# Performance work log

Measured on AMD Instinct MI355X. Metric: run time of the kernel, lower is better.

Reference implementation:

```python
import jax, jax.numpy as jnp
import numpy as np

B, T, C = 4, 1024, 1024
HS = 64
H = C // HS
D_W, D_A, D_V, D_G = 64, 64, 32, 128
EPS = 0.00064  # GroupNorm eps from the module


def _wkv(r, w, k, v, a, b):
    # RWKV-7 recurrence: S_t = S_{t-1}*diag(exp(-exp(w_t))) + (S_{t-1} a_t) b_t^T + v_t k_t^T ; y_t = S_t r_t
    Bv, Tv, Cv = r.shape
    rs = lambda t: t.reshape(Bv, Tv, H, HS)
    r, k, v, a, b = rs(r), rs(k), rs(v), rs(a), rs(b)
    wd = jnp.exp(-jnp.exp(rs(w)))  # per-head per-channel decay in (0,1)

    def step(S, xs):
        r_, w_, k_, v_, a_, b_ = xs  # each (B,H,N)
        sa = jnp.einsum('bhij,bhj->bhi', S, a_)
        S = S * w_[:, :, None, :] + sa[..., None] * b_[:, :, None, :] + v_[..., None] * k_[:, :, None, :]
        y = jnp.einsum('bhij,bhj->bhi', S, r_)
        return S, y

    xs = tuple(jnp.swapaxes(t, 0, 1) for t in (r, wd, k, v, a, b))  # (T,B,H,N)
    S0 = jnp.zeros((Bv, H, HS, HS), r.dtype)
    _, ys = jax.lax.scan(step, S0, xs)
    return jnp.swapaxes(ys, 0, 1).reshape(Bv, Tv, Cv)


def _forward(x, x_r, x_w, x_k, x_v, x_a, x_g, w0, w1, w2, a0, a1, a2, v0, v1, v2,
             g1, g2, k_k, k_a, r_k, Wr, Wk, Wv, Wo, ln_w, ln_b):
    Bv, Tv, Cv = x.shape
    # time_shift(x) - x  (ZeroPad2d((0,0,1,-1)))
    xx = jnp.concatenate([jnp.zeros_like(x[:, :1]), x[:, :-1]], axis=1) - x
    xr = x + xx * x_r; xw = x + xx * x_w; xk = x + xx * x_k
    xv = x + xx * x_v; xa = x + xx * x_a; xg = x + xx * x_g
    r = xr @ Wr
    w = -jax.nn.softplus(-(w0 + jnp.tanh(xw @ w1) @ w2)) - 0.5
    k = xk @ Wk
    v = xv @ Wv
    v_first = jax.lax.stop_gradient(v)  # first layer call: v_first == v.detach()
    v = v + (v_first - v) * jax.nn.sigmoid(v0 + xv @ v1 @ v2)
    a = jax.nn.sigmoid(a0 + xa @ a1 @ a2)
    g = jax.nn.sigmoid(xg @ g1) @ g2
    kk = k * k_k
    kkh = kk.reshape(Bv, Tv, H, HS)
    kkh = kkh / jnp.maximum(jnp.linalg.norm(kkh, axis=-1, keepdims=True), 1e-12)  # F.normalize
    kk = kkh.reshape(Bv, Tv, Cv)
    k = k * (1 + (a - 1) * k_a)
    y = _wkv(r, w, k, v, -kk, kk * a)
    # GroupNorm(H groups, eps=0.00064) over flattened (B*T, C)
    yh = y.reshape(Bv, Tv, H, HS)
    mu = jnp.mean(yh, axis=-1, keepdims=True)
    var = jnp.var(yh, axis=-1, keepdims=True)
    y = ((yh - mu) / jnp.sqrt(var + EPS)).reshape(Bv, Tv, Cv) * ln_w + ln_b
    rt = (r.reshape(Bv, Tv, H, HS) * k.reshape(Bv, Tv, H, HS) * r_k).sum(-1, keepdims=True) * v.reshape(Bv, Tv, H, HS)
    y = y + rt.reshape(Bv, Tv, Cv)
    return (y * g) @ Wo


def setup_inputs():
    key = jax.random.key(0)
    ks = jax.random.split(key, 28)
    it = iter(range(28))
    n = lambda shape, std: jax.random.normal(ks[next(it)], shape, jnp.float32) * std
    s = C ** -0.5
    return {
        'x': n((B, T, C), 1.0),
        'x_r': n((1, 1, C), 0.01), 'x_w': n((1, 1, C), 0.01), 'x_k': n((1, 1, C), 0.01),
        'x_v': n((1, 1, C), 0.01), 'x_a': n((1, 1, C), 0.01), 'x_g': n((1, 1, C), 0.01),
        'w0': n((1, 1, C), 0.02), 'w1': n((C, D_W), 0.04), 'w2': n((D_W, C), 0.04),
        'a0': n((1, 1, C), 0.02), 'a1': n((C, D_A), 0.04), 'a2': n((D_A, C), 0.04),
        'v0': n((1, 1, C), 0.02), 'v1': n((C, D_V), 0.04), 'v2': n((D_V, C), 0.04),
        'g1': n((C, D_G), 0.04), 'g2': n((D_G, C), 0.04),
        'k_k': n((1, 1, C), 0.02), 'k_a': n((1, 1, C), 0.02),
        'r_k': n((H, HS), 0.1) + 0.1 * jnp.arange(H, dtype=jnp.float32)[:, None],
        'Wr': n((C, C), s), 'Wk': n((C, C), s), 'Wv': n((C, C), s), 'Wo': n((C, C), s),
        'ln_w': jnp.ones((C,), jnp.float32), 'ln_b': jnp.zeros((C,), jnp.float32),
    }


def reference(x, x_r, x_w, x_k, x_v, x_a, x_g, w0, w1, w2, a0, a1, a2, v0, v1, v2,
              g1, g2, k_k, k_a, r_k, Wr, Wk, Wv, Wo, ln_w, ln_b):
    return _forward(x, x_r, x_w, x_k, x_v, x_a, x_g, w0, w1, w2, a0, a1, a2,
                    v0, v1, v2, g1, g2, k_k, k_a, r_k, Wr, Wk, Wv, Wo, ln_w, ln_b)
```

## Files before the change

kernel.cpp:

```cpp
#include <hip/hip_runtime.h>
#include <math.h>

#define Bsz 4
#define Tt  1024
#define Cc  1024
#define Hh  16
#define HSs 64
#define CL  32
#define NCH (Tt / CL)
#define STRD 260

typedef __attribute__((ext_vector_type(8))) short bf16x8;
typedef __attribute__((ext_vector_type(4))) float f32x4;

__device__ __forceinline__ float sigf(float x) { return 1.f / (1.f + expf(-x)); }

__device__ __forceinline__ unsigned short f2bf(float f) {
    unsigned int u = __float_as_uint(f);
    u = u + 0x7fffu + ((u >> 16) & 1u);
    return (unsigned short)(u >> 16);
}
__device__ __forceinline__ float bf2f(unsigned short u) {
    return __uint_as_float(((unsigned int)u) << 16);
}
__device__ __forceinline__ float dpp_add_xor1(float x) {
    int y = __builtin_amdgcn_mov_dpp(__float_as_int(x), 0xB1, 0xF, 0xF, true);
    return x + __int_as_float(y);
}
__device__ __forceinline__ float dpp_add_xor2(float x) {
    int y = __builtin_amdgcn_mov_dpp(__float_as_int(x), 0x4E, 0xF, 0xF, true);
    return x + __int_as_float(y);
}

__device__ __forceinline__ void gload16(const void* g, void* l) {
    __builtin_amdgcn_global_load_lds(
        (const __attribute__((address_space(1))) unsigned int*)g,
        (__attribute__((address_space(3))) unsigned int*)l, 16, 0, 0);
}

__device__ __forceinline__ void tcast64(
    const float* __restrict__ W, unsigned short* __restrict__ WT,
    int K, int N, int n0, int k0, int tid, unsigned short tile[64][68])
{
    const int tr = tid >> 4, tc4 = (tid & 15) * 4;
#pragma unroll
    for (int s = 0; s < 4; ++s) {
        int kk = tr + s * 16;
        float4 w4 = *(const float4*)(W + (size_t)(k0 + kk) * N + n0 + tc4);
        tile[kk][tc4 + 0] = f2bf(w4.x);
        tile[kk][tc4 + 1] = f2bf(w4.y);
        tile[kk][tc4 + 2] = f2bf(w4.z);
        tile[kk][tc4 + 3] = f2bf(w4.w);
    }
    __syncthreads();
#pragma unroll
    for (int s = 0; s < 4; ++s) {
        int nn = tr + s * 16;
        ushort4 o4;
        o4.x = tile[tc4 + 0][nn];
        o4.y = tile[tc4 + 1][nn];
        o4.z = tile[tc4 + 2][nn];
        o4.w = tile[tc4 + 3][nn];
        *(ushort4*)(WT + (size_t)(n0 + nn) * K + k0 + tc4) = o4;
    }
}

__global__ __launch_bounds__(256) void prep_all(
    const float* __restrict__ x, const float* __restrict__ x_r,
    const float* __restrict__ x_k, const float* __restrict__ x_v,
    const float* __restrict__ Wr, const float* __restrict__ Wk,
    const float* __restrict__ Wv, const float* __restrict__ Wo,
// ... 34 lines not shown
        for (int j = 0; j < 4; ++j) {
            float xx = xpf[j] - xcf[j];
            rp[j] = f2bf(xcf[j] + xx * mrf[j]);
            kp[j] = f2bf(xcf[j] + xx * mkf[j]);
            vp[j] = f2bf(xcf[j] + xx * mvf[j]);
        }
        *(ushort4*)(xr + o + c0) = r4;
        *(ushort4*)(xk + o + c0) = k4;
        *(ushort4*)(xvo + o + c0) = v4;
        return;
    }
    bid -= 4096;
    if (bid < 1024) {
        int which = bid >> 8, id0 = bid & 255;
        const float* W = which == 0 ? Wr : which == 1 ? Wk : which == 2 ? Wv : Wo;
        unsigned short* WT = which == 0 ? WrT : which == 1 ? WkT : which == 2 ? WvT : WoT;
        tcast64(W, WT, Cc, Cc, (id0 & 15) * 64, (id0 >> 4) * 64, tid, tile);
        return;
    }
    bid -= 1024;
    if (bid < 16) { tcast64(w1, w1t, Cc, 64, 0, bid * 64, tid, tile); return; }
    bid -= 16;
    if (bid < 16) { tcast64(a1, a1t, Cc, 64, 0, bid * 64, tid, tile); return; }
    bid -= 16;
    if (bid < 32) { tcast64(g1, g1t, Cc, 128, (bid & 1) * 64, (bid >> 1) * 64, tid, tile); return; }
    bid -= 32;
    if (bid < 16) { tcast64(w2, w2t, 64, Cc, bid * 64, 0, tid, tile); return; }
    bid -= 16;
    if (bid < 16) { tcast64(a2, a2t, 64, Cc, bid * 64, 0, tid, tile); return; }
    bid -= 16;
    tcast64(g2, g2t, 128, Cc, (bid & 15) * 64, (bid >> 4) * 64, tid, tile);
}

__global__ __launch_bounds__(256) void gemm_rkv(
    const unsigned short* __restrict__ xr, const unsigned short* __restrict__ xk,
    const unsigned short* __restrict__ xv,
    const unsigned short* __restrict__ WrT, const unsigned short* __restrict__ WkT,
    const unsigned short* __restrict__ WvT,
    unsigned short* __restrict__ rbh, float* __restrict__ kb, float* __restrict__ vb)
{
    const int z = blockIdx.z;
    const unsigned short* A  = z == 0 ? xr : z == 1 ? xk : xv;
    const unsigned short* WT = z == 0 ? WrT : z == 1 ? WkT : WvT;
    const int K = Cc, N = Cc;

    __shared__ __attribute__((aligned(16))) unsigned short As[128 * 32];
    __shared__ __attribute__((aligned(16))) unsigned short Bs[128 * 32];
    const int row0 = blockIdx.y * 128;
    const int col0 = blockIdx.x * 128;
    const int tid = threadIdx.x;
    const int wave = tid >> 6, lane = tid & 63;
    const int wr = wave >> 1, wc = wave & 1;
    const int lr = lane & 15, lk = lane >> 4;

    f32x4 acc[4][4];
#pragma unroll
    for (int m = 0; m < 4; ++m)
#pragma unroll
        for (int n = 0; n < 4; ++n)
#pragma unroll
            for (int r = 0; r < 4; ++r) acc[m][n][r] = 0.f;

    const int lrow = lane >> 2;
    const int lcol8 = (lane & 3) * 8;

    for (int k0 = 0; k0 < K; k0 += 32) {
#pragma unroll
        for (int e = 0; e < 2; ++e) {
            int cib = wave * 128 + e * 64;
            int row = (cib >> 2) + lrow;
            gload16(A  + (size_t)(row0 + row) * K + k0 + lcol8, &As[cib * 8]);
            gload16(WT + (size_t)(col0 + row) * K + k0 + lcol8, &Bs[cib * 8]);
        }
        __syncthreads();
        bf16x8 af[4], bff[4];
#pragma unroll
        for (int m = 0; m < 4; ++m)
            af[m] = *(const bf16x8*)&As[(wr * 64 + m * 16 + lr) * 32 + lk * 8];
#pragma unroll
        for (int n = 0; n < 4; ++n)
            bff[n] = *(const bf16x8*)&Bs[(wc * 64 + n * 16 + lr) * 32 + lk * 8];
#pragma unroll
        for (int m = 0; m < 4; ++m)
#pragma unroll
            for (int n = 0; n < 4; ++n)
                acc[m][n] = __builtin_amdgcn_mfma_f32_16x16x32_bf16(af[m], bff[n], acc[m][n], 0, 0, 0);
        __syncthreads();
    }

#pragma unroll
    for (int m = 0; m < 4; ++m)
#pragma unroll
        for (int n = 0; n < 4; ++n) {
            int col = col0 + wc * 64 + n * 16 + lr;
#pragma unroll
            for (int r = 0; r < 4; ++r) {
                int row = row0 + wr * 64 + m * 16 + lk * 4 + r;
                if (z == 0) rbh[(size_t)row * N + col] = f2bf(acc[m][n][r]);
                else if (z == 1) kb[(size_t)row * N + col] = acc[m][n][r];
                else vb[(size_t)row * N + col] = acc[m][n][r];
            }
        }
}

__global__ __launch_bounds__(256) void gemm_bf16(
    const unsigned short* __restrict__ A, const unsigned short* __restrict__ WT,
    float* __restrict__ out, int M, int N, int K)
{
    __shared__ __attribute__((aligned(16))) unsigned short As[128 * 32];
    __shared__ __attribute__((aligned(16))) unsigned short Bs[128 * 32];
    const int row0 = blockIdx.y * 128;
    const int col0 = blockIdx.x * 128;
    const int tid = threadIdx.x;
    const int wave = tid >> 6, lane = tid & 63;
    const int wr = wave >> 1, wc = wave & 1;
    const int lr = lane & 15, lk = lane >> 4;

    f32x4 acc[4][4];
#pragma unroll
    for (int m = 0; m < 4; ++m)
#pragma unroll
        for (int n = 0; n < 4; ++n)
#pragma unroll
            for (int r = 0; r < 4; ++r) acc[m][n][r] = 0.f;

    const int lrow = lane >> 2;
    const int lcol8 = (lane & 3) * 8;

    for (int k0 = 0; k0 < K; k0 += 32) {
#pragma unroll
        for (int e = 0; e < 2; ++e) {
            int cib = wave * 128 + e * 64;
            int row = (cib >> 2) + lrow;
            gload16(A  + (size_t)(row0 + row) * K + k0 + lcol8, &As[cib * 8]);
            gload16(WT + (size_t)(col0 + row) * K + k0 + lcol8, &Bs[cib * 8]);
        }
        __syncthreads();
        bf16x8 af[4], bff[4];
#pragma unroll
        for (int m = 0; m < 4; ++m)
            af[m] = *(const bf16x8*)&As[(wr * 64 + m * 16 + lr) * 32 + lk * 8];
#pragma unroll
        for (int n = 0; n < 4; ++n)
            bff[n] = *(const bf16x8*)&Bs[(wc * 64 + n * 16 + lr) * 32 + lk * 8];
#pragma unroll
        for (int m = 0; m < 4; ++m)
#pragma unroll
            for (int n = 0; n < 4; ++n)
                acc[m][n] = __builtin_amdgcn_mfma_f32_16x16x32_bf16(af[m], bff[n], acc[m][n], 0, 0, 0);
        __syncthreads();
    }

#pragma unroll
    for (int m = 0; m < 4; ++m)
#pragma unroll
        for (int n = 0; n < 4; ++n) {
            int col = col0 + wc * 64 + n * 16 + lr;
#pragma unroll
            for (int r = 0; r < 4; ++r) {
                int row = row0 + wr * 64 + m * 16 + lk * 4 + r;
                out[(size_t)row * N + col] = acc[m][n][r];
            }
        }
}

__global__ __launch_bounds__(256) void lowrank1_fused(
    const float* __restrict__ x,
    const float* __restrict__ x_w, const float* __restrict__ x_a,
    const float* __restrict__ x_g,
    const unsigned short* __restrict__ w1t, const unsigned short* __restrict__ a1t,
    const unsigned short* __restrict__ g1t,
    unsigned short* __restrict__ hw, unsigned short* __restrict__ ha,
    unsigned short* __restrict__ hg)
{
    const int seg = blockIdx.x;
    const float* mix; const unsigned short* WT; unsigned short* out;
    int N, col0, epi;
    if (seg == 0)      { mix = x_w; WT = w1t; out = hw; N = 64;  col0 = 0; epi = 1; }
    else if (seg == 1) { mix = x_a; WT = a1t; out = ha; N = 64;  col0 = 0; epi = 0; }
    else               { mix = x_g; WT = g1t; out = hg; N = 128; col0 = (seg - 2) * 64; epi = 2; }

    __shared__ __attribute__((aligned(16))) unsigned short As[128][40];
    __shared__ __attribute__((aligned(16))) unsigned short Bs[64][40];
    const int row0 = blockIdx.y * 128;
    const int tid = threadIdx.x;
    const int wave = tid >> 6, lane = tid & 63;
    const int lr = lane & 15, lk = lane >> 4;

    f32x4 acc[2][4];
#pragma unroll
    for (int m = 0; m < 2; ++m)
#pragma unroll
        for (int n = 0; n < 4; ++n)
#pragma unroll
            for (int r = 0; r < 4; ++r) acc[m][n][r] = 0.f;

    for (int k0 = 0; k0 < Cc; k0 += 32) {
#pragma unroll
        for (int e = 0; e < 2; ++e) {
            int idx = tid * 2 + e;
            int ar = idx >> 2, ac = (idx & 3) * 8;
            int row = row0 + ar;
            const float* xp = x + (size_t)row * Cc + k0 + ac;
            float4 c0 = *(const float4*)xp;
            float4 c1 = *(const float4*)(xp + 4);
            float4 p0, p1;
            if (row & (Tt - 1)) {
                p0 = *(const float4*)(xp - Cc);
                p1 = *(const float4*)(xp - Cc + 4);
            } else {
                p0.x = p0.y = p0.z = p0.w = 0.f;
                p1.x = p1.y = p1.z = p1.w = 0.f;
            }
            float4 m0 = *(const float4*)(mix + k0 + ac);
            float4 m1 = *(const float4*)(mix + k0 + ac + 4);
            const float* cf0 = (const float*)&c0; const float* cf1 = (const float*)&c1;
            const float* pf0 = (const float*)&p0; const float* pf1 = (const float*)&p1;
            const float* mf0 = (const float*)&m0; const float* mf1 = (const float*)&m1;
            ushort4 u0, u1;
            unsigned short* up0 = (unsigned short*)&u0;
            unsigned short* up1 = (unsigned short*)&u1;
#pragma unroll
            for (int j = 0; j < 4; ++j) {
                up0[j] = f2bf(cf0[j] + (pf0[j] - cf0[j]) * mf0[j]);
                up1[j] = f2bf(cf1[j] + (pf1[j] - cf1[j]) * mf1[j]);
            }
            *(ushort4*)&As[ar][ac] = u0;
            *(ushort4*)&As[ar][ac + 4] = u1;
        }
        {
            int br = tid >> 2, bc = (tid & 3) * 8;
            *(uint4*)&Bs[br][bc] = *(const uint4*)(WT + (size_t)(col0 + br) * Cc + k0 + bc);
        }
        __syncthreads();
        bf16x8 af[2], bff[4];
#pragma unroll
        for (int m = 0; m < 2; ++m)
            af[m] = *(const bf16x8*)&As[wave * 32 + m * 16 + lr][lk * 8];
#pragma unroll
        for (int n = 0; n < 4; ++n)
            bff[n] = *(const bf16x8*)&Bs[n * 16 + lr][lk * 8];
#pragma unroll
        for (int m = 0; m < 2; ++m)
#pragma unroll
            for (int n = 0; n < 4; ++n)
                acc[m][n] = __builtin_amdgcn_mfma_f32_16x16x32_bf16(af[m], bff[n], acc[m][n], 0, 0, 0);
        __syncthreads();
    }

#pragma unroll
    for (int m = 0; m < 2; ++m)
#pragma unroll
        for (int n = 0; n < 4; ++n) {
            int col = col0 + n * 16 + lr;
#pragma unroll
            for (int r = 0; r < 4; ++r) {
                int row = row0 + wave * 32 + m * 16 + lk * 4 + r;
                float v = acc[m][n][r];
                if (epi == 1) v = tanhf(v);
                else if (epi == 2) v = sigf(v);
                out[(size_t)row * N + col] = f2bf(v);
            }
        }
}

__global__ __launch_bounds__(256) void stage2_fused(
    const unsigned short* __restrict__ hw, const unsigned short* __restrict__ ha,
    const unsigned short* __restrict__ hg,
    const unsigned short* __restrict__ w2t, const unsigned short* __restrict__ a2t,
    const unsigned short* __restrict__ g2t,
    unsigned short* __restrict__ wdbh, float* __restrict__ ab,
    unsigned short* __restrict__ gb,
    const float* __restrict__ w0, const float* __restrict__ a0)
{
    const int z = blockIdx.z;
    const unsigned short* A  = z == 0 ? hw : z == 1 ? ha : hg;
    const unsigned short* WT = z == 0 ? w2t : z == 1 ? a2t : g2t;
    const float* bias = z == 0 ? w0 : z == 1 ? a0 : nullptr;
    const int K = (z == 2) ? 128 : 64;
    const int N = Cc;

    __shared__ __attribute__((aligned(16))) unsigned short As[128 * 32];
    __shared__ __attribute__((aligned(16))) unsigned short Bs[64 * 32];
    const int row0 = blockIdx.y * 128;
    const int col0 = blockIdx.x * 64;
    const int tid = threadIdx.x;
    const int wave = tid >> 6, lane = tid & 63;
    const int lr = lane & 15, lk = lane >> 4;

    f32x4 acc[2][4];
#pragma unroll
    for (int m = 0; m < 2; ++m)
#pragma unroll
        for (int n = 0; n < 4; ++n)
// ... 24 lines not shown
        for (int n = 0; n < 4; ++n)
            bff[n] = *(const bf16x8*)&Bs[(n * 16 + lr) * 32 + lk * 8];
#pragma unroll
        for (int m = 0; m < 2; ++m)
#pragma unroll
            for (int n = 0; n < 4; ++n)
                acc[m][n] = __builtin_amdgcn_mfma_f32_16x16x32_bf16(af[m], bff[n], acc[m][n], 0, 0, 0);
        __syncthreads();
    }

#pragma unroll
    for (int m = 0; m < 2; ++m)
#pragma unroll
        for (int n = 0; n < 4; ++n) {
            int col = col0 + n * 16 + lr;
#pragma unroll
            for (int r = 0; r < 4; ++r) {
                int row = row0 + wave * 32 + m * 16 + lk * 4 + r;
                float v = acc[m][n][r];
                if (bias) v += bias[col];
                if (z == 0) {
                    v = expf(-0.60653065971263342f * sigf(v));
                    wdbh[(size_t)row * N + col] = f2bf(v);
                } else if (z == 1) {
                    ab[(size_t)row * N + col] = sigf(v);
                } else {
                    gb[(size_t)row * N + col] = f2bf(v);
                }
            }
        }
}

__global__ __launch_bounds__(256) void prep_k_kernel(
    const float* kraw, const float* __restrict__ a,
    const float* __restrict__ k_k, const float* __restrict__ k_a,
    float* kout, unsigned short* __restrict__ aah, unsigned short* __restrict__ bbh)
{
    const int row = blockIdx.x;
    const int tid = threadIdx.x;
    const int c0 = tid * 4;
    const size_t o = (size_t)row * Cc;

    float4 kr = *(const float4*)(kraw + o + c0);
    float4 kkw = *(const float4*)(k_k + c0);
    float4 av = *(const float4*)(a + o + c0);
    float4 kaw = *(const float4*)(k_a + c0);

    float kk[4] = { kr.x * kkw.x, kr.y * kkw.y, kr.z * kkw.z, kr.w * kkw.w };
    float ssq = kk[0]*kk[0] + kk[1]*kk[1] + kk[2]*kk[2] + kk[3]*kk[3];
    ssq += __shfl_xor(ssq, 1);
    ssq += __shfl_xor(ssq, 2);
    ssq += __shfl_xor(ssq, 4);
    ssq += __shfl_xor(ssq, 8);
    float inv = 1.f / fmaxf(sqrtf(ssq), 1e-12f);

    float krr[4] = { kr.x, kr.y, kr.z, kr.w };
    float av4[4] = { av.x, av.y, av.z, av.w };
    float ka4[4] = { kaw.x, kaw.y, kaw.z, kaw.w };
    ushort4 aa4, bb4;
    unsigned short* aap = (unsigned short*)&aa4;
    unsigned short* bbp = (unsigned short*)&bb4;
    float4 kf4;
    float* kfp = (float*)&kf4;
#pragma unroll
    for (int j = 0; j < 4; ++j) {
        float kkn = kk[j] * inv;
        aap[j] = f2bf(-kkn);
        bbp[j] = f2bf(kkn * av4[j]);
        kfp[j] = krr[j] * (1.f + (av4[j] - 1.f) * ka4[j]);
    }
    *(ushort4*)(aah + o + c0) = aa4;
    *(ushort4*)(bbh + o + c0) = bb4;
    *(float4*)(kout + o + c0) = kf4;
}

__global__ __launch_bounds__(256, 1) void wkv_chunk1(
    const unsigned short* __restrict__ rbh, const unsigned short* __restrict__ wdbh,
    const float* __restrict__ kb,
    const unsigned short* __restrict__ aah, const unsigned short* __restrict__ bbh,
    unsigned short* __restrict__ TLt,
    unsigned short* __restrict__ Rho,
    unsigned short* __restrict__ ZLt,
    unsigned short* __restrict__ Alh)
{
    __shared__ float st[CL * STRD];
    __shared__ float A_l[CL][CL + 1];
    const int blk = blockIdx.x;
    const int bh = blk >> 5;
    const int c  = blk & (NCH - 1);
    const int b = bh >> 4, h = bh & 15;
    const size_t base = (size_t)b * Tt * Cc + h * HSs + (size_t)c * CL * Cc;
    const int tid = threadIdx.x;

    {
        const unsigned short* srcs[4] = { aah, wdbh, bbh, rbh };
        const int s = tid >> 3, j8 = (tid & 7) * 8;
#pragma unroll
        for (int arr = 0; arr < 4; ++arr) {
            uint4 u = *(const uint4*)(srcs[arr] + base + (size_t)s * Cc + j8);
            const unsigned int* q = (const unsigned int*)&u;
            float4 f0, f1;
            f0.x = __uint_as_float(q[0] << 16); f0.y = __uint_as_float(q[0] & 0xFFFF0000u);
            f0.z = __uint_as_float(q[1] << 16); f0.w = __uint_as_float(q[1] & 0xFFFF0000u);
            f1.x = __uint_as_float(q[2] << 16); f1.y = __uint_as_float(q[2] & 0xFFFF0000u);
            f1.z = __uint_as_float(q[3] << 16); f1.w = __uint_as_float(q[3] & 0xFFFF0000u);
            *(float4*)&st[s * STRD + arr * 64 + j8] = f0;
            *(float4*)&st[s * STRD + arr * 64 + j8 + 4] = f1;
        }
    }
    __syncthreads();

// ... 49 lines not shown
                    T[rr][4 + e]  = fmaf(T[rr][4 + e],  w[4 + e],  ta[rr] * bv[4 + e]);
                    T[rr][8 + e]  = fmaf(T[rr][8 + e],  w[8 + e],  ta[rr] * bv[8 + e]);
                    T[rr][12 + e] = fmaf(T[rr][12 + e], w[12 + e], ta[rr] * bv[12 + e]);
                    q0 = fmaf(T[rr][e], r[e], q0);
                    q1 = fmaf(T[rr][4 + e], r[4 + e], q1);
                    q2 = fmaf(T[rr][8 + e], r[8 + e], q2);
                    q3 = fmaf(T[rr][12 + e], r[12 + e], q3);
                }
                rp[rr] = (q0 + q1) + (q2 + q3);
            }
#pragma unroll
            for (int rr = 0; rr < 2; ++rr) {
                rp[rr] = dpp_add_xor1(rp[rr]);
                rp[rr] = dpp_add_xor2(rp[rr]);
            }
            if (jc == 0) {
                ushort2 o2;
                o2.x = f2bf(rp[0]); o2.y = f2bf(rp[1]);
                *(ushort2*)(Rho + rhob + t * 64 + i0) = o2;
            }
        }
        const size_t tlb = (size_t)blk * 4096;
#pragma unroll
        for (int cc = 0; cc < 16; ++cc) {
            ushort2 o2;
            o2.x = f2bf(T[0][cc]); o2.y = f2bf(T[1][cc]);
            *(ushort2*)(TLt + tlb + (size_t)(j0 + cc) * 64 + i0) = o2;
        }
    } else {
        const int idx2 = (wv - 2) * 64 + lane;
        const int s = idx2 >> 2, q4 = idx2 & 3;
        const int j0 = q4 * 16;
        float kreg[16];
#pragma unroll
        for (int q = 0; q < 4; ++q)
            *(float4*)&kreg[q * 4] = *(const float4*)(kb + base + (size_t)s * Cc + j0 + q * 4);
        float z[16];
#pragma unroll
        for (int u = 0; u < 16; ++u) z[u] = 0.f;

        for (int t = 0; t < CL; ++t) {
            const float* sp = st + t * STRD;
            float a[16], w[16], bv[16], r[16];
#pragma unroll
            for (int q = 0; q < 4; ++q) {
                *(float4*)&a[q * 4]  = *(const float4*)(sp + 0 * 64 + j0 + q * 4);
                *(float4*)&w[q * 4]  = *(const float4*)(sp + 1 * 64 + j0 + q * 4);
                *(float4*)&bv[q * 4] = *(const float4*)(sp + 2 * 64 + j0 + q * 4);
                *(float4*)&r[q * 4]  = *(const float4*)(sp + 3 * 64 + j0 + q * 4);
            }
            float q0 = z[0] * a[0], q1 = z[4] * a[4];
            float q2 = z[8] * a[8], q3 = z[12] * a[12];
#pragma unroll
            for (int e = 1; e < 4; ++e) {
                q0 = fmaf(z[e], a[e], q0);
                q1 = fmaf(z[4 + e], a[4 + e], q1);
                q2 = fmaf(z[8 + e], a[8 + e], q2);
                q3 = fmaf(z[12 + e], a[12 + e], q3);
            }
            float za = (q0 + q1) + (q2 + q3);
            za = dpp_add_xor1(za);
            za = dpp_add_xor2(za);
#pragma unroll
            for (int u = 0; u < 16; ++u)
                z[u] = fmaf(z[u], w[u], za * bv[u]);
            if (s == t) {
#pragma unroll
                for (int u = 0; u < 16; ++u) z[u] = kreg[u];
            }
// ... 5 lines not shown
                p1 = fmaf(z[4 + e], r[4 + e], p1);
                p2 = fmaf(z[8 + e], r[8 + e], p2);
                p3 = fmaf(z[12 + e], r[12 + e], p3);
            }
            float al = (p0 + p1) + (p2 + p3);
            al = dpp_add_xor1(al);
            al = dpp_add_xor2(al);
            if (q4 == 0) A_l[t][s] = al;
        }
        const size_t zlb = (size_t)blk * (CL * 64);
#pragma unroll
        for (int u = 0; u < 16; ++u)
            ZLt[zlb + (size_t)(j0 + u) * 32 + s] = f2bf(z[u]);
    }
    __syncthreads();

    if (tid < 128) {
        const int t = tid >> 2, s8 = (tid & 3) * 8;
        ushort4 o0, o1;
        unsigned short* p0 = (unsigned short*)&o0;
        unsigned short* p1 = (unsigned short*)&o1;
#pragma unroll
        for (int e = 0; e < 4; ++e) {
            p0[e] = f2bf(A_l[t][s8 + e]);
            p1[e] = f2bf(A_l[t][s8 + 4 + e]);
        }
        unsigned short* dst = Alh + (size_t)blk * 1024 + t * 32 + s8;
        *(ushort4*)dst = o0;
        *(ushort4*)(dst + 4) = o1;
    }
}

__global__ __launch_bounds__(256, 1) void wkv_chunk2(
    const float* __restrict__ vb, const unsigned short* __restrict__ TLt,
    const unsigned short* __restrict__ Rho, const unsigned short* __restrict__ ZLt,
    const unsigned short* __restrict__ Alh, float* __restrict__ yb)
{
    __shared__ unsigned short Sl[64 * 72];
    __shared__ unsigned short Ttl[64 * 72];
    __shared__ unsigned short Ztl[64 * 40];
    __shared__ unsigned short Rl[32 * 72];
    __shared__ unsigned short Vtl[64 * 40];
    __shared__ unsigned short All[32 * 40];
    const int bh = blockIdx.x;
    const size_t vbase = (size_t)(bh >> 4) * Tt * Cc + (bh & 15) * HSs;
    const int tid = threadIdx.x;
    const int wv = tid >> 6, lane = tid & 63;
    const int lr = lane & 15, lk = lane >> 4;
    const int i0w = wv * 16;

    f32x4 S[4];
#pragma unroll
    for (int n = 0; n < 4; ++n)
#pragma unroll
        for (int r = 0; r < 4; ++r) S[n][r] = 0.f;

    uint4 pT0, pT1, pZ, pR, pAl;
    float4 pV0, pV1;
    const int vs = tid >> 3, vi0 = (tid & 7) * 8;

#define C2_LOAD(c_) do { \
    size_t cb_ = (size_t)(bh * NCH + (c_)); \
    const uint4* tp_ = (const uint4*)(TLt + cb_ * 4096); \
    pT0 = tp_[tid * 2]; pT1 = tp_[tid * 2 + 1]; \
    pZ = ((const uint4*)(ZLt + cb_ * 2048))[tid]; \
    pR = ((const uint4*)(Rho + cb_ * 2048))[tid]; \
    if (tid < 128) pAl = ((const uint4*)(Alh + cb_ * 1024))[tid]; \
    const float* vp_ = vb + vbase + (size_t)((c_) * CL + vs) * Cc + vi0; \
    pV0 = *(const float4*)vp_; pV1 = *(const float4*)(vp_ + 4); \
} while (0)

#define C2_STORE() do { \
    *(uint4*)&Ttl[(tid >> 2) * 72 + (tid & 3) * 16] = pT0; \
    *(uint4*)&Ttl[(tid >> 2) * 72 + (tid & 3) * 16 + 8] = pT1; \
    *(uint4*)&Ztl[(tid >> 2) * 40 + (tid & 3) * 8] = pZ; \
    *(uint4*)&Rl[(tid >> 3) * 72 + (tid & 7) * 8] = pR; \
    if (tid < 128) *(uint4*)&All[(tid >> 2) * 40 + (tid & 3) * 8] = pAl; \
    const float* pv_ = (const float*)&pV0; \
    Vtl[(vi0 + 0) * 40 + vs] = f2bf(pv_[0]); \
    Vtl[(vi0 + 1) * 40 + vs] = f2bf(pv_[1]); \
    Vtl[(vi0 + 2) * 40 + vs] = f2bf(pv_[2]); \
    Vtl[(vi0 + 3) * 40 + vs] = f2bf(pv_[3]); \
    const float* pw_ = (const float*)&pV1; \
    Vtl[(vi0 + 4) * 40 + vs] = f2bf(pw_[0]); \
    Vtl[(vi0 + 5) * 40 + vs] = f2bf(pw_[1]); \
    Vtl[(vi0 + 6) * 40 + vs] = f2bf(pw_[2]); \
    Vtl[(vi0 + 7) * 40 + vs] = f2bf(pw_[3]); \
} while (0)

    C2_LOAD(0);
    for (int c = 0; c < NCH; ++c) {
        __syncthreads();
#pragma unroll
        for (int n = 0; n < 4; ++n) {
#pragma unroll
            for (int r = 0; r < 4; ++r)
                Sl[(i0w + lk * 4 + r) * 72 + n * 16 + lr] = f2bf(S[n][r]);
        }
        C2_STORE();
        if (c + 1 < NCH) C2_LOAD(c + 1);
        __syncthreads();

        bf16x8 sA0 = *(const bf16x8*)&Sl[(i0w + lr) * 72 + lk * 8];
        bf16x8 sA1 = *(const bf16x8*)&Sl[(i0w + lr) * 72 + 32 + lk * 8];
        bf16x8 vA = *(const bf16x8*)&Vtl[(i0w + lr) * 40 + lk * 8];

#pragma unroll
        for (int nt = 0; nt < 2; ++nt) {
            int t = nt * 16 + lr;
            float* yp = yb + vbase + (size_t)(c * CL + t) * Cc + i0w + lk * 4;
            f32x4 yc = { 0.f, 0.f, 0.f, 0.f };
            bf16x8 b0 = *(const bf16x8*)&Rl[t * 72 + lk * 8];
            bf16x8 b1 = *(const bf16x8*)&Rl[t * 72 + 32 + lk * 8];
            bf16x8 al8 = *(const bf16x8*)&All[t * 40 + lk * 8];
            yc = __builtin_amdgcn_mfma_f32_16x16x32_bf16(sA0, b0, yc, 0, 0, 0);
            yc = __builtin_amdgcn_mfma_f32_16x16x32_bf16(sA1, b1, yc, 0, 0, 0);
            yc = __builtin_amdgcn_mfma_f32_16x16x32_bf16(vA, al8, yc, 0, 0, 0);
            *(f32x4*)yp = yc;
        }

#pragma unroll
        for (int n = 0; n < 4; ++n) {
            int j = n * 16 + lr;
            bf16x8 t0 = *(const bf16x8*)&Ttl[j * 72 + lk * 8];
            bf16x8 t1 = *(const bf16x8*)&Ttl[j * 72 + 32 + lk * 8];
            bf16x8 z0 = *(const bf16x8*)&Ztl[j * 40 + lk * 8];
            f32x4 acc = { 0.f, 0.f, 0.f, 0.f };
            acc = __builtin_amdgcn_mfma_f32_16x16x32_bf16(sA0, t0, acc, 0, 0, 0);
            acc = __builtin_amdgcn_mfma_f32_16x16x32_bf16(sA1, t1, acc, 0, 0, 0);
            acc = __builtin_amdgcn_mfma_f32_16x16x32_bf16(vA, z0, acc, 0, 0, 0);
            S[n] = acc;
        }
    }
#undef C2_LOAD
#undef C2_STORE
}

__global__ __launch_bounds__(256) void gn_rt_kernel(
    const float* __restrict__ yb, const unsigned short* __restrict__ rbh,
    const float* __restrict__ kb, const float* __restrict__ vb,
    const unsigned short* __restrict__ gb, const float* __restrict__ r_k,
    const float* __restrict__ ln_w, const float* __restrict__ ln_b,
    unsigned short* __restrict__ zb)
{
    const int row = blockIdx.x;
    const int tid = threadIdx.x;
    const int c0 = tid * 4;
    const int hd = tid >> 4;
    const int n0 = c0 & 63;
    const size_t o = (size_t)row * Cc;

    float4 y4 = *(const float4*)(yb + o + c0);
    ushort4 r4u = *(const ushort4*)(rbh + o + c0);
    float4 k4 = *(const float4*)(kb + o + c0);
    float4 v4 = *(const float4*)(vb + o + c0);
    ushort4 g4u = *(const ushort4*)(gb + o + c0);
    float4 rk4 = *(const float4*)(r_k + hd * 64 + n0);

    float yv[4] = { y4.x, y4.y, y4.z, y4.w };
    float rv[4] = { bf2f(r4u.x), bf2f(r4u.y), bf2f(r4u.z), bf2f(r4u.w) };
    float kv[4] = { k4.x, k4.y, k4.z, k4.w };
    float vv[4] = { v4.x, v4.y, v4.z, v4.w };
    float gv[4] = { bf2f(g4u.x), bf2f(g4u.y), bf2f(g4u.z), bf2f(g4u.w) };
    float rkv[4] = { rk4.x, rk4.y, rk4.z, rk4.w };

    float sum = 0.f, ssq = 0.f, dot = 0.f;
#pragma unroll
    for (int j = 0; j < 4; ++j) {
        sum += yv[j];
        ssq += yv[j] * yv[j];
        dot += rv[j] * kv[j] * rkv[j];
    }
#pragma unroll
    for (int m = 1; m <= 8; m <<= 1) {
        sum += __shfl_xor(sum, m);
        ssq += __shfl_xor(ssq, m);
        dot += __shfl_xor(dot, m);
    }
    const float mu = sum * (1.f / 64.f);
    const float var = ssq * (1.f / 64.f) - mu * mu;
    const float inv = rsqrtf(var + 0.00064f);

    ushort4 z4;
    unsigned short* zp = (unsigned short*)&z4;
#pragma unroll
    for (int j = 0; j < 4; ++j) {
        int c = c0 + j;
        float yg = (yv[j] - mu) * inv * ln_w[c] + ln_b[c];
        yg += dot * vv[j];
        zp[j] = f2bf(yg * gv[j]);
    }
    *(ushort4*)(zb + o + c0) = z4;
}


// ... 4 lines not shown
    const float* x   = (const float*)d_in[0];
    const float* x_r = (const float*)d_in[1];
    const float* x_w = (const float*)d_in[2];
    const float* x_k = (const float*)d_in[3];
    const float* x_v = (const float*)d_in[4];
    const float* x_a = (const float*)d_in[5];
    const float* x_g = (const float*)d_in[6];
    const float* w0  = (const float*)d_in[7];
    const float* w1  = (const float*)d_in[8];
    const float* w2  = (const float*)d_in[9];
    const float* a0  = (const float*)d_in[10];
    const float* a1  = (const float*)d_in[11];
    const float* a2  = (const float*)d_in[12];
    const float* g1  = (const float*)d_in[16];
    const float* g2  = (const float*)d_in[17];
    const float* k_k = (const float*)d_in[18];
    const float* k_a = (const float*)d_in[19];
    const float* r_k = (const float*)d_in[20];
    const float* Wr  = (const float*)d_in[21];
    const float* Wk  = (const float*)d_in[22];
    const float* Wv  = (const float*)d_in[23];
    const float* Wo  = (const float*)d_in[24];
    const float* ln_w = (const float*)d_in[25];
    const float* ln_b = (const float*)d_in[26];

    float* ws = (float*)d_ws;
    const size_t S = (size_t)Bsz * Tt * Cc;
    const int M = Bsz * Tt;

    unsigned short* rbh = (unsigned short*)(ws + 0 * S);
    unsigned short* zb  = (unsigned short*)ws + S;
    unsigned short* wdbh = (unsigned short*)(ws + 1 * S);
    unsigned short* gb  = (unsigned short*)(ws + 1 * S) + S;
    float* kb  = ws + 2 * S;
    float* vb  = ws + 3 * S;
    unsigned short* aah = (unsigned short*)(ws + 4 * S);
    unsigned short* bbh = (unsigned short*)(ws + 4 * S) + S;
    float* yb  = ws + 5 * S;
    unsigned short* xr = (unsigned short*)(ws + 6 * S);
    unsigned short* xk = (unsigned short*)(ws + 6 * S) + S;
    unsigned short* Rho = xr;
    unsigned short* ZLt = xk;
    unsigned short* xv = (unsigned short*)(ws + 7 * S);
    unsigned short* hw = xv + S;
    unsigned short* ha = hw + 262144;
    unsigned short* hg = ha + 262144;
    unsigned short* w1t = hg + 524288;
    unsigned short* a1t = w1t + 65536;
    unsigned short* g1t = a1t + 65536;
    unsigned short* w2t = g1t + 131072;
    unsigned short* a2t = w2t + 65536;
    unsigned short* g2t = a2t + 65536;
    unsigned short* WrT = (unsigned short*)(ws + 8 * S);
    unsigned short* WkT = WrT + 1048576;
    unsigned short* WvT = WkT + 1048576;
    unsigned short* WoT = WvT + 1048576;
    unsigned short* Alh = WoT + 1048576;
    float* ab = ws + 9 * S;
    unsigned short* TLt = (unsigned short*)(ws + 9 * S);

    dim3 blk(256);

    prep_all<<<dim3(4096 + 1024 + 128), blk, 0, stream>>>(
        x, x_r, x_k, x_v, Wr, Wk, Wv, Wo, w1, a1, g1, w2, a2, g2,
        xr, xk, xv, WrT, WkT, WvT, WoT, w1t, a1t, g1t, w2t, a2t, g2t);

    lowrank1_fused<<<dim3(4, 32), blk, 0, stream>>>(x, x_w, x_a, x_g, w1t, a1t, g1t, hw, ha, hg);

    gemm_rkv<<<dim3(8, 32, 3), blk, 0, stream>>>(xr, xk, xv, WrT, WkT, WvT, rbh, kb, vb);

    stage2_fused<<<dim3(16, 32, 3), blk, 0, stream>>>(hw, ha, hg, w2t, a2t, g2t, wdbh, ab, gb, w0, a0);

    prep_k_kernel<<<dim3(M), blk, 0, stream>>>(kb, ab, k_k, k_a, kb, aah, bbh);

    wkv_chunk1<<<dim3(64 * NCH), dim3(256), 0, stream>>>(rbh, wdbh, kb, aah, bbh, TLt, Rho, ZLt, Alh);
    wkv_chunk2<<<dim3(64), blk, 0, stream>>>(vb, TLt, Rho, ZLt, Alh, yb);

    gn_rt_kernel<<<dim3(M), blk, 0, stream>>>(yb, rbh, kb, vb, gb, r_k, ln_w, ln_b, zb);

    gemm_bf16<<<dim3(8, 32), blk, 0, stream>>>(zb, WoT, (float*)d_out, M, Cc, Cc);
}
```

Before: 278.0 us.

## Store k and v in bf16 and fuse low-rank stage-1 into RKV GEMM launch

The k and v projections are now stored as bf16 instead of fp32. Every consumer (prep_k, both wkv chunk kernels, the groupnorm kernel) now reads and unpacks bf16, which halves that memory traffic and removes the fp32-to-bf16 conversion when v is staged. The separate low-rank first-stage kernel is merged into the RKV GEMM as an extra grid z-slice that shares LDS, saving a launch and letting the two workloads run concurrently. The cost is reduced precision of k and v in the recurrence and normalization, plus many idle blocks in the extra slice that exit immediately.

```diff
diff --git a/kernel.cpp b/kernel.cpp
--- a/kernel.cpp
+++ b/kernel.cpp
@@ -37,6 +37,15 @@
         (const __attribute__((address_space(1))) unsigned int*)g,
         (__attribute__((address_space(3))) unsigned int*)l, 16, 0, 0);
 }
+
+#define UNPK8(dst, u4, off) do { \
+    const unsigned int* q_ = (const unsigned int*)&(u4); \
+    _Pragma("unroll") \
+    for (int e_ = 0; e_ < 4; ++e_) { \
+        (dst)[(off) + 2 * e_]     = __uint_as_float(q_[e_] << 16); \
+        (dst)[(off) + 2 * e_ + 1] = __uint_as_float(q_[e_] & 0xFFFF0000u); \
+    } \
+} while (0)
 
 __device__ __forceinline__ void tcast64(
     const float* __restrict__ W, unsigned short* __restrict__ WT,
@@ -137,139 +146,13 @@
     tcast64(g2, g2t, 128, Cc, (bid & 15) * 64, (bid >> 4) * 64, tid, tile);
 }
 
-__global__ __launch_bounds__(256) void gemm_rkv(
+__global__ __launch_bounds__(256) void mid_fused(
     const unsigned short* __restrict__ xr, const unsigned short* __restrict__ xk,
     const unsigned short* __restrict__ xv,
     const unsigned short* __restrict__ WrT, const unsigned short* __restrict__ WkT,
     const unsigned short* __restrict__ WvT,
-    unsigned short* __restrict__ rbh, float* __restrict__ kb, float* __restrict__ vb)
-{
-    const int z = blockIdx.z;
-    const unsigned short* A  = z == 0 ? xr : z == 1 ? xk : xv;
-    const unsigned short* WT = z == 0 ? WrT : z == 1 ? WkT : WvT;
-    const int K = Cc, N = Cc;
-
-    __shared__ __attribute__((aligned(16))) unsigned short As[128 * 32];
-    __shared__ __attribute__((aligned(16))) unsigned short Bs[128 * 32];
-    const int row0 = blockIdx.y * 128;
-    const int col0 = blockIdx.x * 128;
-    const int tid = threadIdx.x;
-    const int wave = tid >> 6, lane = tid & 63;
-    const int wr = wave >> 1, wc = wave & 1;
-    const int lr = lane & 15, lk = lane >> 4;
-
-    f32x4 acc[4][4];
-#pragma unroll
-    for (int m = 0; m < 4; ++m)
-#pragma unroll
-        for (int n = 0; n < 4; ++n)
-#pragma unroll
-            for (int r = 0; r < 4; ++r) acc[m][n][r] = 0.f;
-
-    const int lrow = lane >> 2;
-    const int lcol8 = (lane & 3) * 8;
-
-    for (int k0 = 0; k0 < K; k0 += 32) {
-#pragma unroll
-        for (int e = 0; e < 2; ++e) {
-            int cib = wave * 128 + e * 64;
-            int row = (cib >> 2) + lrow;
-            gload16(A  + (size_t)(row0 + row) * K + k0 + lcol8, &As[cib * 8]);
-            gload16(WT + (size_t)(col0 + row) * K + k0 + lcol8, &Bs[cib * 8]);
-        }
-        __syncthreads();
-        bf16x8 af[4], bff[4];
-#pragma unroll
-        for (int m = 0; m < 4; ++m)
-            af[m] = *(const bf16x8*)&As[(wr * 64 + m * 16 + lr) * 32 + lk * 8];
-#pragma unroll
-        for (int n = 0; n < 4; ++n)
-            bff[n] = *(const bf16x8*)&Bs[(wc * 64 + n * 16 + lr) * 32 + lk * 8];
-#pragma unroll
-        for (int m = 0; m < 4; ++m)
-#pragma unroll
-            for (int n = 0; n < 4; ++n)
-                acc[m][n] = __builtin_amdgcn_mfma_f32_16x16x32_bf16(af[m], bff[n], acc[m][n], 0, 0, 0);
-        __syncthreads();
-    }
-
-#pragma unroll
-    for (int m = 0; m < 4; ++m)
-#pragma unroll
-        for (int n = 0; n < 4; ++n) {
-            int col = col0 + wc * 64 + n * 16 + lr;
-#pragma unroll
-            for (int r = 0; r < 4; ++r) {
-                int row = row0 + wr * 64 + m * 16 + lk * 4 + r;
-                if (z == 0) rbh[(size_t)row * N + col] = f2bf(acc[m][n][r]);
-                else if (z == 1) kb[(size_t)row * N + col] = acc[m][n][r];
-                else vb[(size_t)row * N + col] = acc[m][n][r];
-            }
-        }
-}
-
-__global__ __launch_bounds__(256) void gemm_bf16(
-    const unsigned short* __restrict__ A, const unsigned short* __restrict__ WT,
-    float* __restrict__ out, int M, int N, int K)
-{
-    __shared__ __attribute__((aligned(16))) unsigned short As[128 * 32];
-    __shared__ __attribute__((aligned(16))) unsigned short Bs[128 * 32];
-    const int row0 = blockIdx.y * 128;
-    const int col0 = blockIdx.x * 128;
-    const int tid = threadIdx.x;
-    const int wave = tid >> 6, lane = tid & 63;
-    const int wr = wave >> 1, wc = wave & 1;
-    const int lr = lane & 15, lk = lane >> 4;
-
-    f32x4 acc[4][4];
-#pragma unroll
-    for (int m = 0; m < 4; ++m)
-#pragma unroll
-        for (int n = 0; n < 4; ++n)
-#pragma unroll
-            for (int r = 0; r < 4; ++r) acc[m][n][r] = 0.f;
-
-    const int lrow = lane >> 2;
-    const int lcol8 = (lane & 3) * 8;
-
-    for (int k0 = 0; k0 < K; k0 += 32) {
-#pragma unroll
-        for (int e = 0; e < 2; ++e) {
-            int cib = wave * 128 + e * 64;
-            int row = (cib >> 2) + lrow;
-            gload16(A  + (size_t)(row0 + row) * K + k0 + lcol8, &As[cib * 8]);
-            gload16(WT + (size_t)(col0 + row) * K + k0 + lcol8, &Bs[cib * 8]);
-        }
-        __syncthreads();
-        bf16x8 af[4], bff[4];
-#pragma unroll
-        for (int m = 0; m < 4; ++m)
-            af[m] = *(const bf16x8*)&As[(wr * 64 + m * 16 + lr) * 32 + lk * 8];
-#pragma unroll
-        for (int n = 0; n < 4; ++n)
-            bff[n] = *(const bf16x8*)&Bs[(wc * 64 + n * 16 + lr) * 32 + lk * 8];
-#pragma unroll
-        for (int m = 0; m < 4; ++m)
-#pragma unroll
-            for (int n = 0; n < 4; ++n)
-                acc[m][n] = __builtin_amdgcn_mfma_f32_16x16x32_bf16(af[m], bff[n], acc[m][n], 0, 0, 0);
-        __syncthreads();
-    }
-
-#pragma unroll
-    for (int m = 0; m < 4; ++m)
-#pragma unroll
-        for (int n = 0; n < 4; ++n) {
-            int col = col0 + wc * 64 + n * 16 + lr;
-#pragma unroll
-            for (int r = 0; r < 4; ++r) {
-                int row = row0 + wr * 64 + m * 16 + lk * 4 + r;
-                out[(size_t)row * N + col] = acc[m][n][r];
-            }
-        }
-}
-
-__global__ __launch_bounds__(256) void lowrank1_fused(
+    unsigned short* __restrict__ rbh, unsigned short* __restrict__ kbh,
+    unsigned short* __restrict__ vbh,
     const float* __restrict__ x,
     const float* __restrict__ x_w, const float* __restrict__ x_a,
     const float* __restrict__ x_g,
@@ -278,6 +161,73 @@
     unsigned short* __restrict__ hw, unsigned short* __restrict__ ha,
     unsigned short* __restrict__ hg)
 {
+    __shared__ __attribute__((aligned(16))) unsigned short smem[16384];
+    const int z = blockIdx.z;
+    const int tid = threadIdx.x;
+    const int wave = tid >> 6, lane = tid & 63;
+    const int lr = lane & 15, lk = lane >> 4;
+
+    if (z < 3) {
+        const unsigned short* A  = z == 0 ? xr : z == 1 ? xk : xv;
+        const unsigned short* WT = z == 0 ? WrT : z == 1 ? WkT : WvT;
+        unsigned short* outh = z == 0 ? rbh : z == 1 ? kbh : vbh;
+        const int K = Cc, N = Cc;
+        unsigned short* As = smem;
+        unsigned short* Bs = smem + 4096;
+        const int row0 = blockIdx.y * 128;
+        const int col0 = blockIdx.x * 128;
+        const int wr = wave >> 1, wc = wave & 1;
+
+        f32x4 acc[4][4];
+#pragma unroll
+        for (int m = 0; m < 4; ++m)
+#pragma unroll
+            for (int n = 0; n < 4; ++n)
+#pragma unroll
+                for (int r = 0; r < 4; ++r) acc[m][n][r] = 0.f;
+
+        const int lrow = lane >> 2;
+        const int lcol8 = (lane & 3) * 8;
+
+        for (int k0 = 0; k0 < K; k0 += 32) {
+#pragma unroll
+            for (int e = 0; e < 2; ++e) {
+                int cib = wave * 128 + e * 64;
+                int row = (cib >> 2) + lrow;
+                gload16(A  + (size_t)(row0 + row) * K + k0 + lcol8, &As[cib * 8]);
+                gload16(WT + (size_t)(col0 + row) * K + k0 + lcol8, &Bs[cib * 8]);
+            }
+            __syncthreads();
+            bf16x8 af[4], bff[4];
+#pragma unroll
+            for (int m = 0; m < 4; ++m)
+                af[m] = *(const bf16x8*)&As[(wr * 64 + m * 16 + lr) * 32 + lk * 8];
+#pragma unroll
+            for (int n = 0; n < 4; ++n)
+                bff[n] = *(const bf16x8*)&Bs[(wc * 64 + n * 16 + lr) * 32 + lk * 8];
+#pragma unroll
+            for (int m = 0; m < 4; ++m)
+#pragma unroll
+                for (int n = 0; n < 4; ++n)
+                    acc[m][n] = __builtin_amdgcn_mfma_f32_16x16x32_bf16(af[m], bff[n], acc[m][n], 0, 0, 0);
+            __syncthreads();
+        }
+
+#pragma unroll
+        for (int m = 0; m < 4; ++m)
+#pragma unroll
+            for (int n = 0; n < 4; ++n) {
+                int col = col0 + wc * 64 + n * 16 + lr;
+#pragma unroll
+                for (int r = 0; r < 4; ++r) {
+                    int row = row0 + wr * 64 + m * 16 + lk * 4 + r;
+                    outh[(size_t)row * N + col] = f2bf(acc[m][n][r]);
+                }
+            }
+        return;
+    }
+
+    if (blockIdx.x >= 4) return;
     const int seg = blockIdx.x;
     const float* mix; const unsigned short* WT; unsigned short* out;
     int N, col0, epi;
@@ -285,12 +235,9 @@
     else if (seg == 1) { mix = x_a; WT = a1t; out = ha; N = 64;  col0 = 0; epi = 0; }
     else               { mix = x_g; WT = g1t; out = hg; N = 128; col0 = (seg - 2) * 64; epi = 2; }
 
-    __shared__ __attribute__((aligned(16))) unsigned short As[128][40];
-    __shared__ __attribute__((aligned(16))) unsigned short Bs[64][40];
+    unsigned short (*As40)[40] = (unsigned short(*)[40])smem;
+    unsigned short (*Bs40)[40] = (unsigned short(*)[40])(smem + 5120);
     const int row0 = blockIdx.y * 128;
-    const int tid = threadIdx.x;
-    const int wave = tid >> 6, lane = tid & 63;
-    const int lr = lane & 15, lk = lane >> 4;
 
     f32x4 acc[2][4];
 #pragma unroll
@@ -330,21 +277,21 @@
                 up0[j] = f2bf(cf0[j] + (pf0[j] - cf0[j]) * mf0[j]);
                 up1[j] = f2bf(cf1[j] + (pf1[j] - cf1[j]) * mf1[j]);
             }
-            *(ushort4*)&As[ar][ac] = u0;
-            *(ushort4*)&As[ar][ac + 4] = u1;
+            *(ushort4*)&As40[ar][ac] = u0;
+            *(ushort4*)&As40[ar][ac + 4] = u1;
         }
         {
             int br = tid >> 2, bc = (tid & 3) * 8;
-            *(uint4*)&Bs[br][bc] = *(const uint4*)(WT + (size_t)(col0 + br) * Cc + k0 + bc);
+            *(uint4*)&Bs40[br][bc] = *(const uint4*)(WT + (size_t)(col0 + br) * Cc + k0 + bc);
         }
         __syncthreads();
         bf16x8 af[2], bff[4];
 #pragma unroll
         for (int m = 0; m < 2; ++m)
-            af[m] = *(const bf16x8*)&As[wave * 32 + m * 16 + lr][lk * 8];
+            af[m] = *(const bf16x8*)&As40[wave * 32 + m * 16 + lr][lk * 8];
 #pragma unroll
         for (int n = 0; n < 4; ++n)
-            bff[n] = *(const bf16x8*)&Bs[n * 16 + lr][lk * 8];
+            bff[n] = *(const bf16x8*)&Bs40[n * 16 + lr][lk * 8];
 #pragma unroll
         for (int m = 0; m < 2; ++m)
 #pragma unroll
@@ -365,6 +312,67 @@
                 if (epi == 1) v = tanhf(v);
                 else if (epi == 2) v = sigf(v);
                 out[(size_t)row * N + col] = f2bf(v);
+            }
+        }
+}
+
+__global__ __launch_bounds__(256) void gemm_bf16(
+    const unsigned short* __restrict__ A, const unsigned short* __restrict__ WT,
+    float* __restrict__ out, int M, int N, int K)
+{
+    __shared__ __attribute__((aligned(16))) unsigned short As[128 * 32];
+    __shared__ __attribute__((aligned(16))) unsigned short Bs[128 * 32];
+    const int row0 = blockIdx.y * 128;
+    const int col0 = blockIdx.x * 128;
+    const int tid = threadIdx.x;
+    const int wave = tid >> 6, lane = tid & 63;
+    const int wr = wave >> 1, wc = wave & 1;
+    const int lr = lane & 15, lk = lane >> 4;
+
+    f32x4 acc[4][4];
+#pragma unroll
+    for (int m = 0; m < 4; ++m)
+#pragma unroll
+        for (int n = 0; n < 4; ++n)
+#pragma unroll
+            for (int r = 0; r < 4; ++r) acc[m][n][r] = 0.f;
+
+    const int lrow = lane >> 2;
+    const int lcol8 = (lane & 3) * 8;
+
+    for (int k0 = 0; k0 < K; k0 += 32) {
+#pragma unroll
+        for (int e = 0; e < 2; ++e) {
+            int cib = wave * 128 + e * 64;
+            int row = (cib >> 2) + lrow;
+            gload16(A  + (size_t)(row0 + row) * K + k0 + lcol8, &As[cib * 8]);
+            gload16(WT + (size_t)(col0 + row) * K + k0 + lcol8, &Bs[cib * 8]);
+        }
+        __syncthreads();
+        bf16x8 af[4], bff[4];
+#pragma unroll
+        for (int m = 0; m < 4; ++m)
+            af[m] = *(const bf16x8*)&As[(wr * 64 + m * 16 + lr) * 32 + lk * 8];
+#pragma unroll
+        for (int n = 0; n < 4; ++n)
+            bff[n] = *(const bf16x8*)&Bs[(wc * 64 + n * 16 + lr) * 32 + lk * 8];
+#pragma unroll
+        for (int m = 0; m < 4; ++m)
+#pragma unroll
+            for (int n = 0; n < 4; ++n)
+                acc[m][n] = __builtin_amdgcn_mfma_f32_16x16x32_bf16(af[m], bff[n], acc[m][n], 0, 0, 0);
+        __syncthreads();
+    }
+
+#pragma unroll
+    for (int m = 0; m < 4; ++m)
+#pragma unroll
+        for (int n = 0; n < 4; ++n) {
+            int col = col0 + wc * 64 + n * 16 + lr;
+#pragma unroll
+            for (int r = 0; r < 4; ++r) {
+                int row = row0 + wr * 64 + m * 16 + lk * 4 + r;
+                out[(size_t)row * N + col] = acc[m][n][r];
             }
         }
 }
@@ -455,21 +463,25 @@
 }
 
 __global__ __launch_bounds__(256) void prep_k_kernel(
-    const float* kraw, const float* __restrict__ a,
+    unsigned short* kio, const float* __restrict__ a,
     const float* __restrict__ k_k, const float* __restrict__ k_a,
-    float* kout, unsigned short* __restrict__ aah, unsigned short* __restrict__ bbh)
+    unsigned short* __restrict__ aah, unsigned short* __restrict__ bbh)
 {
     const int row = blockIdx.x;
     const int tid = threadIdx.x;
     const int c0 = tid * 4;
     const size_t o = (size_t)row * Cc;
 
-    float4 kr = *(const float4*)(kraw + o + c0);
+    ushort4 kr4u = *(const ushort4*)(kio + o + c0);
     float4 kkw = *(const float4*)(k_k + c0);
     float4 av = *(const float4*)(a + o + c0);
     float4 kaw = *(const float4*)(k_a + c0);
 
-    float kk[4] = { kr.x * kkw.x, kr.y * kkw.y, kr.z * kkw.z, kr.w * kkw.w };
+    float krr[4] = { bf2f(kr4u.x), bf2f(kr4u.y), bf2f(kr4u.z), bf2f(kr4u.w) };
+    const float* kkwf = (const float*)&kkw;
+    float kk[4];
+#pragma unroll
+    for (int j = 0; j < 4; ++j) kk[j] = krr[j] * kkwf[j];
     float ssq = kk[0]*kk[0] + kk[1]*kk[1] + kk[2]*kk[2] + kk[3]*kk[3];
     ssq += __shfl_xor(ssq, 1);
     ssq += __shfl_xor(ssq, 2);
@@ -477,29 +489,27 @@
     ssq += __shfl_xor(ssq, 8);
     float inv = 1.f / fmaxf(sqrtf(ssq), 1e-12f);
 
-    float krr[4] = { kr.x, kr.y, kr.z, kr.w };
     float av4[4] = { av.x, av.y, av.z, av.w };
     float ka4[4] = { kaw.x, kaw.y, kaw.z, kaw.w };
-    ushort4 aa4, bb4;
+    ushort4 aa4, bb4, kf4;
     unsigned short* aap = (unsigned short*)&aa4;
     unsigned short* bbp = (unsigned short*)&bb4;
-    float4 kf4;
-    float* kfp = (float*)&kf4;
+    unsigned short* kfp = (unsigned short*)&kf4;
 #pragma unroll
     for (int j = 0; j < 4; ++j) {
         float kkn = kk[j] * inv;
         aap[j] = f2bf(-kkn);
         bbp[j] = f2bf(kkn * av4[j]);
-        kfp[j] = krr[j] * (1.f + (av4[j] - 1.f) * ka4[j]);
+        kfp[j] = f2bf(krr[j] * (1.f + (av4[j] - 1.f) * ka4[j]));
     }
     *(ushort4*)(aah + o + c0) = aa4;
     *(ushort4*)(bbh + o + c0) = bb4;
-    *(float4*)(kout + o + c0) = kf4;
+    *(ushort4*)(kio + o + c0) = kf4;
 }
 
 __global__ __launch_bounds__(256, 1) void wkv_chunk1(
     const unsigned short* __restrict__ rbh, const unsigned short* __restrict__ wdbh,
-    const float* __restrict__ kb,
+    const unsigned short* __restrict__ kbh,
     const unsigned short* __restrict__ aah, const unsigned short* __restrict__ bbh,
     unsigned short* __restrict__ TLt,
     unsigned short* __restrict__ Rho,
@@ -615,9 +625,12 @@
         const int s = idx2 >> 2, q4 = idx2 & 3;
         const int j0 = q4 * 16;
         float kreg[16];
-#pragma unroll
-        for (int q = 0; q < 4; ++q)
-            *(float4*)&kreg[q * 4] = *(const float4*)(kb + base + (size_t)s * Cc + j0 + q * 4);
+        {
+            uint4 u0 = *(const uint4*)(kbh + base + (size_t)s * Cc + j0);
+            uint4 u1 = *(const uint4*)(kbh + base + (size_t)s * Cc + j0 + 8);
+            UNPK8(kreg, u0, 0);
+            UNPK8(kreg, u1, 8);
+        }
         float z[16];
 #pragma unroll
         for (int u = 0; u < 16; ++u) z[u] = 0.f;
@@ -689,7 +702,7 @@
 }
 
 __global__ __launch_bounds__(256, 1) void wkv_chunk2(
-    const float* __restrict__ vb, const unsigned short* __restrict__ TLt,
+    const unsigned short* __restrict__ vbh, const unsigned short* __restrict__ TLt,
     const unsigned short* __restrict__ Rho, const unsigned short* __restrict__ ZLt,
     const unsigned short* __restrict__ Alh, float* __restrict__ yb)
 {
@@ -712,8 +725,7 @@
 #pragma unroll
         for (int r = 0; r < 4; ++r) S[n][r] = 0.f;
 
-    uint4 pT0, pT1, pZ, pR, pAl;
-    float4 pV0, pV1;
+    uint4 pT0, pT1, pZ, pR, pAl, pVu;
     const int vs = tid >> 3, vi0 = (tid & 7) * 8;
 
 #define C2_LOAD(c_) do { \
@@ -723,8 +735,7 @@
     pZ = ((const uint4*)(ZLt + cb_ * 2048))[tid]; \
     pR = ((const uint4*)(Rho + cb_ * 2048))[tid]; \
     if (tid < 128) pAl = ((const uint4*)(Alh + cb_ * 1024))[tid]; \
-    const float* vp_ = vb + vbase + (size_t)((c_) * CL + vs) * Cc + vi0; \
-    pV0 = *(const float4*)vp_; pV1 = *(const float4*)(vp_ + 4); \
+    pVu = *(const uint4*)(vbh + vbase + (size_t)((c_) * CL + vs) * Cc + vi0); \
 } while (0)
 
 #define C2_STORE() do { \
@@ -733,16 +744,15 @@
     *(uint4*)&Ztl[(tid >> 2) * 40 + (tid & 3) * 8] = pZ; \
     *(uint4*)&Rl[(tid >> 3) * 72 + (tid & 7) * 8] = pR; \
     if (tid < 128) *(uint4*)&All[(tid >> 2) * 40 + (tid & 3) * 8] = pAl; \
-    const float* pv_ = (const float*)&pV0; \
-    Vtl[(vi0 + 0) * 40 + vs] = f2bf(pv_[0]); \
-    Vtl[(vi0 + 1) * 40 + vs] = f2bf(pv_[1]); \
-    Vtl[(vi0 + 2) * 40 + vs] = f2bf(pv_[2]); \
-    Vtl[(vi0 + 3) * 40 + vs] = f2bf(pv_[3]); \
-    const float* pw_ = (const float*)&pV1; \
-    Vtl[(vi0 + 4) * 40 + vs] = f2bf(pw_[0]); \
-    Vtl[(vi0 + 5) * 40 + vs] = f2bf(pw_[1]); \
-    Vtl[(vi0 + 6) * 40 + vs] = f2bf(pw_[2]); \
-    Vtl[(vi0 + 7) * 40 + vs] = f2bf(pw_[3]); \
+    const unsigned short* pvu_ = (const unsigned short*)&pVu; \
+    Vtl[(vi0 + 0) * 40 + vs] = pvu_[0]; \
+    Vtl[(vi0 + 1) * 40 + vs] = pvu_[1]; \
+    Vtl[(vi0 + 2) * 40 + vs] = pvu_[2]; \
+    Vtl[(vi0 + 3) * 40 + vs] = pvu_[3]; \
+    Vtl[(vi0 + 4) * 40 + vs] = pvu_[4]; \
+    Vtl[(vi0 + 5) * 40 + vs] = pvu_[5]; \
+    Vtl[(vi0 + 6) * 40 + vs] = pvu_[6]; \
+    Vtl[(vi0 + 7) * 40 + vs] = pvu_[7]; \
 } while (0)
 
     C2_LOAD(0);
@@ -795,7 +805,7 @@
 
 __global__ __launch_bounds__(256) void gn_rt_kernel(
     const float* __restrict__ yb, const unsigned short* __restrict__ rbh,
-    const float* __restrict__ kb, const float* __restrict__ vb,
+    const unsigned short* __restrict__ kbh, const unsigned short* __restrict__ vbh,
     const unsigned short* __restrict__ gb, const float* __restrict__ r_k,
     const float* __restrict__ ln_w, const float* __restrict__ ln_b,
     unsigned short* __restrict__ zb)
@@ -809,15 +819,15 @@
 
     float4 y4 = *(const float4*)(yb + o + c0);
     ushort4 r4u = *(const ushort4*)(rbh + o + c0);
-    float4 k4 = *(const float4*)(kb + o + c0);
-    float4 v4 = *(const float4*)(vb + o + c0);
+    ushort4 k4u = *(const ushort4*)(kbh + o + c0);
+    ushort4 v4u = *(const ushort4*)(vbh + o + c0);
     ushort4 g4u = *(const ushort4*)(gb + o + c0);
     float4 rk4 = *(const float4*)(r_k + hd * 64 + n0);
 
     float yv[4] = { y4.x, y4.y, y4.z, y4.w };
     float rv[4] = { bf2f(r4u.x), bf2f(r4u.y), bf2f(r4u.z), bf2f(r4u.w) };
-    float kv[4] = { k4.x, k4.y, k4.z, k4.w };
-    float vv[4] = { v4.x, v4.y, v4.z, v4.w };
+    float kv[4] = { bf2f(k4u.x), bf2f(k4u.y), bf2f(k4u.z), bf2f(k4u.w) };
+    float vv[4] = { bf2f(v4u.x), bf2f(v4u.y), bf2f(v4u.z), bf2f(v4u.w) };
     float gv[4] = { bf2f(g4u.x), bf2f(g4u.y), bf2f(g4u.z), bf2f(g4u.w) };
     float rkv[4] = { rk4.x, rk4.y, rk4.z, rk4.w };
 
@@ -888,8 +898,8 @@
     unsigned short* zb  = (unsigned short*)ws + S;
     unsigned short* wdbh = (unsigned short*)(ws + 1 * S);
     unsigned short* gb  = (unsigned short*)(ws + 1 * S) + S;
-    float* kb  = ws + 2 * S;
-    float* vb  = ws + 3 * S;
+    unsigned short* kbh = (unsigned short*)(ws + 2 * S);
+    unsigned short* vbh = (unsigned short*)(ws + 2 * S) + S;
     unsigned short* aah = (unsigned short*)(ws + 4 * S);
     unsigned short* bbh = (unsigned short*)(ws + 4 * S) + S;
     float* yb  = ws + 5 * S;
@@ -921,18 +931,18 @@
         x, x_r, x_k, x_v, Wr, Wk, Wv, Wo, w1, a1, g1, w2, a2, g2,
         xr, xk, xv, WrT, WkT, WvT, WoT, w1t, a1t, g1t, w2t, a2t, g2t);
 
-    lowrank1_fused<<<dim3(4, 32), blk, 0, stream>>>(x, x_w, x_a, x_g, w1t, a1t, g1t, hw, ha, hg);
-
-    gemm_rkv<<<dim3(8, 32, 3), blk, 0, stream>>>(xr, xk, xv, WrT, WkT, WvT, rbh, kb, vb);
+    mid_fused<<<dim3(8, 32, 4), blk, 0, stream>>>(
+        xr, xk, xv, WrT, WkT, WvT, rbh, kbh, vbh,
+        x, x_w, x_a, x_g, w1t, a1t, g1t, hw, ha, hg);
 
     stage2_fused<<<dim3(16, 32, 3), blk, 0, stream>>>(hw, ha, hg, w2t, a2t, g2t, wdbh, ab, gb, w0, a0);
 
-    prep_k_kernel<<<dim3(M), blk, 0, stream>>>(kb, ab, k_k, k_a, kb, aah, bbh);
-
-    wkv_chunk1<<<dim3(64 * NCH), dim3(256), 0, stream>>>(rbh, wdbh, kb, aah, bbh, TLt, Rho, ZLt, Alh);
-    wkv_chunk2<<<dim3(64), blk, 0, stream>>>(vb, TLt, Rho, ZLt, Alh, yb);
-
-    gn_rt_kernel<<<dim3(M), blk, 0, stream>>>(yb, rbh, kb, vb, gb, r_k, ln_w, ln_b, zb);
+    prep_k_kernel<<<dim3(M), blk, 0, stream>>>(kbh, ab, k_k, k_a, aah, bbh);
+
+    wkv_chunk1<<<dim3(64 * NCH), dim3(256), 0, stream>>>(rbh, wdbh, kbh, aah, bbh, TLt, Rho, ZLt, Alh);
+    wkv_chunk2<<<dim3(64), blk, 0, stream>>>(vbh, TLt, Rho, ZLt, Alh, yb);
+
+    gn_rt_kernel<<<dim3(M), blk, 0, stream>>>(yb, rbh, kbh, vbh, gb, r_k, ln_w, ln_b, zb);
 
     gemm_bf16<<<dim3(8, 32), blk, 0, stream>>>(zb, WoT, (float*)d_out, M, Cc, Cc);
 }
```

Measured after the change: 278.5 us. Within noise of the previous version (+0.2%).
